# Kernel optimization log

Measured on AMD Instinct MI355X. Metric: run time of the kernel, lower is better.

## Reference

```python
import jax, jax.numpy as jnp
import numpy as np

BATCH, SEQ, EMBED = 8, 1024, 2048
HEADS, LATENT = 16, 512
HEAD_DIM = EMBED // HEADS            # 128
NOPE = HEAD_DIM // 4                 # 32 (qk_rope_dim=96 is even, no adjust)
ROPE_D = HEAD_DIM - NOPE             # 96
THETA = 10000.0


def _rope_tables(seq_len):
    # matches torch: freqs over arange(0, rope_dim, 2)/rope_dim
    freqs = 1.0 / THETA ** (jnp.arange(0, ROPE_D, 2, dtype=jnp.float32) / ROPE_D)
    emb = jnp.arange(seq_len, dtype=jnp.float32)[:, None] * freqs[None, :]  # [S, ROPE_D//2]
    return jnp.cos(emb), jnp.sin(emb)


def _apply_rope(x, cos, sin):
    # x: [B,H,S,D]; cos/sin: [S,D//2]. NOTE: original concatenates halves (non-interleaved output).
    xe, xo = x[..., ::2], x[..., 1::2]
    return jnp.concatenate([xe * cos - xo * sin, xo * cos + xe * sin], axis=-1)


def setup_inputs() -> dict:
    key = jax.random.key(0)
    ks = jax.random.split(key, 5)
    x = jax.random.normal(ks[0], (BATCH, SEQ, EMBED), jnp.float32)
    Wq = jax.random.normal(ks[1], (EMBED, EMBED), jnp.float32) * 0.02
    Wkv_down = jax.random.normal(ks[2], (EMBED, LATENT), jnp.float32) * 0.02
    Wk_up = jax.random.normal(ks[3], (LATENT, EMBED), jnp.float32) * 0.02
    Wv_up = jax.random.normal(ks[4], (LATENT, EMBED), jnp.float32) * 0.02
    return {"x": x, "Wq": Wq, "Wkv_down": Wkv_down, "Wk_up": Wk_up, "Wv_up": Wv_up}


def reference(x, Wq, Wkv_down, Wk_up, Wv_up):
    B, S, E = x.shape
    # projections (weights stored [in, out], equivalent to nn.Linear math)
    q = (x @ Wq).reshape(B, S, HEADS, HEAD_DIM).transpose(0, 2, 1, 3)   # [B,H,S,D]
    q_nope, q_rope = q[..., :NOPE], q[..., NOPE:]
    c_kv = x @ Wkv_down                                                  # [B,S,latent]
    k = (c_kv @ Wk_up).reshape(B, S, HEADS, HEAD_DIM).transpose(0, 2, 1, 3)
    v = (c_kv @ Wv_up).reshape(B, S, HEADS, HEAD_DIM).transpose(0, 2, 1, 3)
    k_nope, k_rope = k[..., :NOPE], k[..., NOPE:]

    cos, sin = _rope_tables(S)
    q_rope = _apply_rope(q_rope, cos, sin)
    k_rope = _apply_rope(k_rope, cos, sin)

    qf = jnp.concatenate([q_nope, q_rope], axis=-1)
    kf = jnp.concatenate([k_nope, k_rope], axis=-1)

    scale = jnp.float32(1.0 / np.sqrt(HEAD_DIM))
    scores = jnp.einsum('bhqd,bhkd->bhqk', qf, kf) * scale
    causal = jnp.triu(jnp.ones((S, S), dtype=bool), k=1)  # past_length=0
    scores = jnp.where(causal, -jnp.inf, scores)
    weights = jax.nn.softmax(scores, axis=-1)
    out = jnp.einsum('bhqk,bhkd->bhqd', weights, v)
    return out.transpose(0, 2, 1, 3).reshape(B, S, E)
```

## Files before the change

### kernel.cpp

```cpp
#include <hip/hip_runtime.h>
#include <stdint.h>

typedef unsigned short u16;
typedef __bf16 bf16x8 __attribute__((ext_vector_type(8)));
typedef float    f32x4 __attribute__((ext_vector_type(4)));
typedef unsigned short u16x8 __attribute__((ext_vector_type(8)));
typedef unsigned short u16x4 __attribute__((ext_vector_type(4)));

#define BB 8
#define SS 1024
#define EE 2048
#define HH 16
#define DD 128

__device__ __forceinline__ u16 f2bf(float f){
  union { float f; unsigned u; } v; v.f = f;
  unsigned r = v.u + 0x7FFFu + ((v.u >> 16) & 1u);
  return (u16)(r >> 16);
}
__device__ __forceinline__ float bf2f(u16 h){
  union { unsigned u; float f; } v; v.u = ((unsigned)h) << 16;
  return v.f;
}
__device__ __forceinline__ bf16x8 ld8(const u16* p){
  return __builtin_bit_cast(bf16x8, *(const u16x8*)p);
}

typedef __attribute__((address_space(1))) const unsigned int gas_u32;
typedef __attribute__((address_space(3))) unsigned int las_u32;
__device__ __forceinline__ void g2l16(const u16* g, u16* l){
  __builtin_amdgcn_global_load_lds((gas_u32*)g, (las_u32*)l, 16, 0, 0);
}

#define BARRIER() asm volatile("s_barrier" ::: "memory")
#define VMC(n)    asm volatile("s_waitcnt vmcnt(" #n ")" ::: "memory")

__global__ __launch_bounds__(256) void cvt_f32_bf16(const float* __restrict__ in,
                                                    u16* __restrict__ out, int n){
  int i = (blockIdx.x*256 + threadIdx.x)*8;
  if (i >= n) return;
  float4 v0 = *(const float4*)(in + i);
  float4 v1 = *(const float4*)(in + i + 4);
  u16x8 o;
  o[0]=f2bf(v0.x); o[1]=f2bf(v0.y); o[2]=f2bf(v0.z); o[3]=f2bf(v0.w);
  o[4]=f2bf(v1.x); o[5]=f2bf(v1.y); o[6]=f2bf(v1.z); o[7]=f2bf(v1.w);
  *(u16x8*)(out + i) = o;
}

__global__ __launch_bounds__(256) void transposeW(const float* __restrict__ W,
                                                  u16* __restrict__ Wt, int K, int N){
  __shared__ float t[32][33];
  int c = threadIdx.x & 31, r = threadIdx.x >> 5;
  int bx = blockIdx.x, by = blockIdx.y;
  #pragma unroll
  for (int i = 0; i < 32; i += 8)
    t[r+i][c] = W[(size_t)(by*32 + r + i)*N + bx*32 + c];
  __syncthreads();
  #pragma unroll
  for (int i = 0; i < 32; i += 8)
    Wt[(size_t)(bx*32 + r + i)*K + by*32 + c] = f2bf(t[c][r+i]);
}

__global__ __launch_bounds__(256) void rope_tables(float* __restrict__ cosb,
                                                   float* __restrict__ sinb){
  int i = blockIdx.x*256 + threadIdx.x;
  if (i >= SS*48) return;
  int s = i / 48, j = i % 48;
  float freq = powf(10000.0f, -((float)(2*j)) / 96.0f);
  float e = (float)s * freq;
  cosb[i] = cosf(e);
  sinb[i] = sinf(e);
}

__global__ __launch_bounds__(256) void rope_apply2(u16* __restrict__ qp,
                                                   u16* __restrict__ kp,
                                                   const float* __restrict__ cosb,
                                                   const float* __restrict__ sinb){
  u16* base = blockIdx.y ? kp : qp;
  int t = blockIdx.x*256 + threadIdx.x;
  int row = t >> 4, h = t & 15, s = row & (SS-1);
  u16* p = base + (size_t)row*EE + h*DD + 32;
  float e[48], o[48];
  #pragma unroll
  for (int c = 0; c < 12; c++){
    u16x8 v = *(const u16x8*)(p + c*8);
    #pragma unroll
    for (int j = 0; j < 4; j++){
      e[c*4 + j] = bf2f(v[2*j]);
      o[c*4 + j] = bf2f(v[2*j+1]);
    }
  }
  u16 ob[96];
  #pragma unroll
  for (int j = 0; j < 48; j++){
    float cs = cosb[s*48 + j], sn = sinb[s*48 + j];
    ob[j]      = f2bf(e[j]*cs - o[j]*sn);
    ob[48 + j] = f2bf(o[j]*cs + e[j]*sn);
  }
  #pragma unroll
  for (int c = 0; c < 12; c++)
    *(u16x8*)(p + c*8) = *(const u16x8*)(ob + c*8);
}

__global__ __launch_bounds__(256) void gemm_bt(const u16* __restrict__ A,
    const u16* __restrict__ Bt, u16* __restrict__ C, int M, int N, int K){
  __shared__ u16 Al[128*32];
  __shared__ u16 Bl[128*32];
  const int tid = threadIdx.x;
  const int lane = tid & 63, w = tid >> 6;
  const int wr = w >> 1, wc = w & 1;
  const int l15 = lane & 15, l4 = lane >> 4;
  const int bm = blockIdx.y*128, bn = blockIdx.x*128;
  const int srow = tid >> 2;
  const int skc  = (tid & 3) * 8;
  const u16* ga = A  + (size_t)(bm + srow)*K + skc;
  const u16* gb = Bt + (size_t)(bn + srow)*K + skc;
  u16* la = Al + w*512;
  u16* lb = Bl + w*512;
  f32x4 acc[4][4] = {};
  for (int k0 = 0; k0 < K; k0 += 32){
    __syncthreads();
    g2l16(ga + k0,          la);
    g2l16(ga + 64*K + k0,   la + 2048);
    g2l16(gb + k0,          lb);
    g2l16(gb + 64*K + k0,   lb + 2048);
    __syncthreads();
    bf16x8 af[4], bfr[4];
    #pragma unroll
    for (int m = 0; m < 4; m++) af[m]  = ld8(Al + (wr*64 + m*16 + l15)*32 + l4*8);
    #pragma unroll
    for (int n = 0; n < 4; n++) bfr[n] = ld8(Bl + (wc*64 + n*16 + l15)*32 + l4*8);
    #pragma unroll
    for (int m = 0; m < 4; m++)
      #pragma unroll
      for (int n = 0; n < 4; n++)
        acc[m][n] = __builtin_amdgcn_mfma_f32_16x16x32_bf16(af[m], bfr[n], acc[m][n], 0, 0, 0);
  }
  #pragma unroll
  for (int m = 0; m < 4; m++)
    #pragma unroll
    for (int n = 0; n < 4; n++)
      #pragma unroll
      for (int r = 0; r < 4; r++){
        int row = bm + wr*64 + m*16 + l4*4 + r;
        int col = bn + wc*64 + n*16 + l15;
        C[(size_t)row*N + col] = f2bf(acc[m][n][r]);
      }
}

#define AFR(buf, mf, ks) ld8(&AL[buf][wr][((mf)*16 + l15)*64 + ((((ks)*4 + l4) ^ r7) << 3)])
#define BFR(buf, nf, ks) ld8(&BL[buf][wc>>1][(((wc&1)*64 + (nf)*16 + l15))*64 + ((((ks)*4 + l4) ^ r7) << 3)])

#define STAGE_A(buf, h, kt) stage2(aRow, (h), (kt), K, &AL[buf][h][0], wj0)
#define STAGE_B(buf, h, kt) stage2(bRow, (h), (kt), K, &BL[buf][h][0], wj0)

__device__ __forceinline__ void stage2(const u16* rowbase, int h, int kt, int K,
                                       u16* lds, int wj0){
  const u16* g = rowbase + (size_t)h*128*K + kt*64;
  g2l16(g,               lds + wj0*512);
  g2l16(g + (size_t)8*K, lds + wj0*512 + 512);
}

#define PHASE(buf, q, LOADB, STAGE, VM) do{                                        \
  bf16x8 a00 = AFR(buf, 2*(q)  , 0);                                              \
  bf16x8 a01 = AFR(buf, 2*(q)  , 1);                                              \
  bf16x8 a10 = AFR(buf, 2*(q)+1, 0);                                              \
  bf16x8 a11 = AFR(buf, 2*(q)+1, 1);                                              \
  if (LOADB){                                                                      \
    _Pragma("unroll")                                                              \
    for (int nf = 0; nf < 4; nf++){ bq[nf][0]=BFR(buf,nf,0); bq[nf][1]=BFR(buf,nf,1); } \
  }                                                                                \
  STAGE;                                                                           \
  if (VM) VMC(4);                                                                  \
  BARRIER();                                                                       \
  __builtin_amdgcn_s_setprio(1);                                                   \
  _Pragma("unroll")                                                                \
  for (int nf = 0; nf < 4; nf++){                                                  \
    acc[2*(q)][nf]   = __builtin_amdgcn_mfma_f32_16x16x32_bf16(a00, bq[nf][0], acc[2*(q)][nf],0,0,0);   \
    acc[2*(q)+1][nf] = __builtin_amdgcn_mfma_f32_16x16x32_bf16(a10, bq[nf][0], acc[2*(q)+1][nf],0,0,0); \
  }                                                                                \
  _Pragma("unroll")                                                                \
  for (int nf = 0; nf < 4; nf++){                                                  \
    acc[2*(q)][nf]   = __builtin_amdgcn_mfma_f32_16x16x32_bf16(a01, bq[nf][1], acc[2*(q)][nf],0,0,0);   \
    acc[2*(q)+1][nf] = __builtin_amdgcn_mfma_f32_16x16x32_bf16(a11, bq[nf][1], acc[2*(q)+1][nf],0,0,0); \
  }                                                                                \
  __builtin_amdgcn_s_setprio(0);                                                   \
  BARRIER();                                                                       \
  __builtin_amdgcn_sched_barrier(0);                                               \
}while(0)

__global__ __launch_bounds__(512, 2) void gemm8(const u16* __restrict__ A,
    const u16* __restrict__ Bt, u16* __restrict__ C0, u16* __restrict__ C1,
    int K, int Nout, int nsplit, int vt){
  __shared__ u16 AL[2][2][128*64];
  __shared__ u16 BL[2][2][128*64];
  const int tid = threadIdx.x, lane = tid & 63, w = tid >> 6;
  const int wr = w >> 2, wc = w & 3;
  const int l15 = lane & 15, l4 = lane >> 4;
  const int r7 = l15 & 7;
  const int bm = blockIdx.y*256, bn = blockIdx.x*256;
  const int wj0 = w*2;
  const int cswz = (lane & 7) ^ (lane >> 3);
  const u16* aRow = A  + (size_t)(bm + wj0*8 + (lane>>3))*K + cswz*8;
  const u16* bRow = Bt + (size_t)(bn + wj0*8 + (lane>>3))*K + cswz*8;

  const int nkt = K >> 6;
  const int niter = nkt >> 1;

  STAGE_A(0, 0, 0); STAGE_A(0, 1, 0);
  STAGE_B(0, 0, 0); STAGE_B(0, 1, 0);
  STAGE_B(1, 0, 1); STAGE_B(1, 1, 1);
  VMC(4);
  BARRIER();

  f32x4 acc[8][4] = {};
  bf16x8 bq[4][2];

  for (int it = 0; it < niter; ++it){
    const int kto = 2*it + 1;
    int kt2 = 2*it + 2; if (kt2 >= nkt) kt2 -= nkt;
    int kt3 = 2*it + 3; if (kt3 >= nkt) kt3 -= nkt;
    PHASE(0, 0, 1, STAGE_A(1, 0, kto), 0);
    PHASE(0, 1, 0, STAGE_A(1, 1, kto), 0);
    PHASE(0, 2, 0, STAGE_B(0, 0, kt2), 0);
    PHASE(0, 3, 0, STAGE_B(0, 1, kt2), 1);
    PHASE(1, 0, 1, STAGE_A(0, 0, kt2), 0);
    PHASE(1, 1, 0, STAGE_A(0, 1, kt2), 0);
    PHASE(1, 2, 0, STAGE_B(1, 0, kt3), 0);
    PHASE(1, 3, 0, STAGE_B(1, 1, kt3), 1);
  }
  asm volatile("s_waitcnt vmcnt(0)" ::: "memory");

  if (vt && bn >= nsplit){
    const int bcol = bn - nsplit;
    #pragma unroll
    for (int mf = 0; mf < 8; mf++)
      #pragma unroll
      for (int nf = 0; nf < 4; nf++){
        int row0 = bm + wr*128 + mf*16 + l4*4;
        int col  = bcol + wc*64 + nf*16 + l15;
        int bh = (row0 >> 10)*16 + (col >> 7);
        int d  = col & 127;
        int s  = row0 & 1023;
        u16x4 pk;
        #pragma unroll
        for (int r = 0; r < 4; r++) pk[r] = f2bf(acc[mf][nf][r]);
        *(u16x4*)(C1 + (((size_t)(bh*128 + d)) << 10) + s) = pk;
      }
  } else {
    u16* Cd = (bn < nsplit) ? C0 : C1;
    const int bcol = (bn < nsplit) ? bn : bn - nsplit;
    #pragma unroll
    for (int mf = 0; mf < 8; mf++)
      #pragma unroll
      for (int nf = 0; nf < 4; nf++)
        #pragma unroll
        for (int r = 0; r < 4; r++){
          int row = bm + wr*128 + mf*16 + l4*4 + r;
          int col = bcol + wc*64 + nf*16 + l15;
          Cd[(size_t)row*Nout + col] = f2bf(acc[mf][nf][r]);
        }
  }
}

#define PLW 40

__global__ __launch_bounds__(512) void attn(const u16* __restrict__ qp,
                                            const u16* __restrict__ kp,
                                            const u16* __restrict__ vpT,
                                            float* __restrict__ out){
  __shared__ u16 Kl[2][64*128];
  __shared__ u16 Vl[2][128*64];
  __shared__ u16 Pl[8][16*PLW];
  const int tid = threadIdx.x, lane = tid & 63, w = tid >> 6;
  const int l15 = lane & 15, l4 = lane >> 4;
  const int qt = 7 - blockIdx.y;
  const int bh = blockIdx.x;
  const int b = bh >> 4, h = bh & 15;
  const int qbase = qt*128;
  const int qmin = qbase + w*16;
  const int qg = qmin + l15;
  const float c = 0.12751920700948998f;
  const float THR = 62.7f;

  const size_t rowq = (size_t)(b*SS + qg)*EE + h*DD;
  bf16x8 qf[4];
  #pragma unroll
  for (int kk = 0; kk < 4; kk++) qf[kk] = ld8(qp + rowq + kk*32 + l4*8);
  #pragma unroll
  for (int kk = 0; kk < 4; kk++) asm volatile("" : "+v"(qf[kk]));

  f32x4 ao[8] = {};
  float mi = -3e38f, li = 0.0f;

  const int ntiles = 2*qt + 2;
  const int vcc = lane & 7;

  #pragma unroll
  for (int q = 0; q < 2; q++){
    int r = w*8 + q*4 + (lane>>4);
    g2l16(kp + (size_t)(b*SS + r)*EE + h*DD + (((lane&15) ^ (r&7))<<3),
          &Kl[0][0] + w*1024 + q*512);
    int d = w*16 + q*8 + (lane>>3);
    g2l16(vpT + (size_t)(bh*DD + d)*SS + ((vcc ^ (d&7))<<3),
          &Vl[0][0] + w*1024 + q*512);
  }

  for (int t = 0; t < ntiles; t++){
    const int kv0 = t*64;
    const int buf = t & 1;
    {
      const int kvn = (t + 1 < ntiles) ? kv0 + 64 : kv0;
      #pragma unroll
      for (int q = 0; q < 2; q++){
        int r = w*8 + q*4 + (lane>>4);
        g2l16(kp + (size_t)(b*SS + kvn + r)*EE + h*DD + (((lane&15) ^ (r&7))<<3),
              &Kl[buf^1][0] + w*1024 + q*512);
        int d = w*16 + q*8 + (lane>>3);
        g2l16(vpT + (size_t)(bh*DD + d)*SS + kvn + ((vcc ^ (d&7))<<3),
              &Vl[buf^1][0] + w*1024 + q*512);
      }
    }
    VMC(4);
    BARRIER();

    if (kv0 <= qmin + 15){
      float sv[4][4];
      __builtin_amdgcn_s_setprio(1);
      #pragma unroll
      for (int nt = 0; nt < 4; nt++){
        f32x4 sacc = {};
        #pragma unroll
        for (int kk = 0; kk < 4; kk++){
          bf16x8 kf = ld8(&Kl[buf][0] + (nt*16 + l15)*128 + (((kk*4 + l4) ^ (l15&7))<<3));
          sacc = __builtin_amdgcn_mfma_f32_16x16x32_bf16(kf, qf[kk], sacc, 0, 0, 0);
        }
        #pragma unroll
        for (int r = 0; r < 4; r++) sv[nt][r] = sacc[r];
      }
      __builtin_amdgcn_s_setprio(0);
      if (kv0 + 63 > qmin){
        #pragma unroll
        for (int nt = 0; nt < 4; nt++)
          #pragma unroll
          for (int r = 0; r < 4; r++){
            int kg = kv0 + nt*16 + l4*4 + r;
            if (kg > qg) sv[nt][r] = -3e38f;
          }
      }
      float mx = sv[0][0];
      #pragma unroll
      for (int nt = 0; nt < 4; nt++)
        #pragma unroll
        for (int r = 0; r < 4; r++) mx = fmaxf(mx, sv[nt][r]);
      mx = fmaxf(mx, __shfl_xor(mx, 16));
      mx = fmaxf(mx, __shfl_xor(mx, 32));
      if (__any(mx > mi + THR)){
        float mnew = fmaxf(mi, mx);
        float alpha = __builtin_amdgcn_exp2f((mi - mnew)*c);
        li *= alpha;
        #pragma unroll
        for (int n8 = 0; n8 < 8; n8++) ao[n8] *= alpha;
        mi = mnew;
      }
      const float mnc = mi*c;
      float pout[4][4];
      float rs = 0.0f;
      #pragma unroll
      for (int nt = 0; nt < 4; nt++)
        #pragma unroll
        for (int r = 0; r < 4; r++){
          float pv = __builtin_amdgcn_exp2f(__builtin_fmaf(sv[nt][r], c, -mnc));
          pout[nt][r] = pv; rs += pv;
        }
      rs += __shfl_xor(rs, 16);
      rs += __shfl_xor(rs, 32);
      li += rs;
      #pragma unroll
      for (int kk = 0; kk < 2; kk++){
        #pragma unroll
        for (int ntl = 0; ntl < 2; ntl++){
          int nt = kk*2 + ntl;
          u16x4 pk;
          #pragma unroll
          for (int r = 0; r < 4; r++) pk[r] = f2bf(pout[nt][r]);
          *(u16x4*)(&Pl[w][l15*PLW + ntl*16 + l4*4]) = pk;
        }
        bf16x8 pa = ld8(&Pl[w][l15*PLW + l4*8]);
        __builtin_amdgcn_s_setprio(1);
        #pragma unroll
        for (int n8 = 0; n8 < 8; n8++){
          bf16x8 vf = ld8(&Vl[buf][0] + (n8*16 + l15)*64 + (((kk*4 + l4) ^ (l15&7))<<3));
          ao[n8] = __builtin_amdgcn_mfma_f32_16x16x32_bf16(vf, pa, ao[n8], 0, 0, 0);
        }
        __builtin_amdgcn_s_setprio(0);
      }
    }
    BARRIER();
  }
  asm volatile("s_waitcnt vmcnt(0)" ::: "memory");

  const float inv = 1.0f / li;
  const size_t orow = (size_t)(b*SS + qg)*EE + h*DD;
  #pragma unroll
  for (int n8 = 0; n8 < 8; n8++){
    f32x4 o = ao[n8]*inv;
    *(float4*)(out + orow + n8*16 + l4*4) = __builtin_bit_cast(float4, o);
  }
}

extern "C" void kernel_launch(void* const* d_in, const int* in_sizes, int n_in,
                              void* d_out, int out_size, void* d_ws, size_t ws_size,
                              hipStream_t stream){
  const float* x    = (const float*)d_in[0];
  const float* Wq   = (const float*)d_in[1];
  const float* Wkvd = (const float*)d_in[2];
  const float* Wku  = (const float*)d_in[3];
  const float* Wvu  = (const float*)d_in[4];
  float* out = (float*)d_out;
  char* ws = (char*)d_ws;

  u16*   xb    = (u16*)  (ws);
  u16*   WqT   = (u16*)  (ws +  33554432);
  u16*   WkvdT = (u16*)  (ws +  41943040);
  u16*   WkuT  = (u16*)  (ws +  44040192);
  u16*   WvuT  = (u16*)  (ws +  46137344);
  float* cosb  = (float*)(ws +  48234496);
  float* sinb  = (float*)(ws +  48431104);
  u16*   qp    = (u16*)  (ws +  48627712);
  u16*   ckv   = (u16*)  (ws +  82182144);
  u16*   kp    = (u16*)  (ws +  90570752);
  u16*   vpT   = (u16*)  (ws + 124125184);

  cvt_f32_bf16<<<(BB*SS*EE)/(256*8), 256, 0, stream>>>(x, xb, BB*SS*EE);
  transposeW<<<dim3(EE/32,  EE/32), 256, 0, stream>>>(Wq,   WqT,   EE,  EE);
  transposeW<<<dim3(512/32, EE/32), 256, 0, stream>>>(Wkvd, WkvdT, EE,  512);
  transposeW<<<dim3(EE/32, 512/32), 256, 0, stream>>>(Wku,  WkuT,  512, EE);
  transposeW<<<dim3(EE/32, 512/32), 256, 0, stream>>>(Wvu,  WvuT,  512, EE);
  rope_tables<<<(SS*48 + 255)/256, 256, 0, stream>>>(cosb, sinb);

  gemm8<<<dim3(EE/256, (BB*SS)/256), 512, 0, stream>>>(xb, WqT, qp, qp, EE, EE, EE, 0);
  gemm_bt<<<dim3(512/128, (BB*SS)/128), 256, 0, stream>>>(xb, WkvdT, ckv, BB*SS, 512, EE);
  gemm8<<<dim3(4096/256, (BB*SS)/256), 512, 0, stream>>>(ckv, WkuT, kp, vpT, 512, EE, EE, 1);

  rope_apply2<<<dim3((BB*SS*HH)/256, 2), 256, 0, stream>>>(qp, kp, cosb, sinb);

  attn<<<dim3(BB*HH, SS/128), 512, 0, stream>>>(qp, kp, vpT, out);
}
```

Baseline: 306.8 us.

## Fuse Q and KV-down projections into one GEMM and triple-buffer A tiles

After: 306.2 us. About the same (-0.2%).

```diff
diff --git a/kernel.cpp b/kernel.cpp
--- a/kernel.cpp
+++ b/kernel.cpp
@@ -102,57 +102,11 @@
     *(u16x8*)(p + c*8) = *(const u16x8*)(ob + c*8);
 }
 
-__global__ __launch_bounds__(256) void gemm_bt(const u16* __restrict__ A,
-    const u16* __restrict__ Bt, u16* __restrict__ C, int M, int N, int K){
-  __shared__ u16 Al[128*32];
-  __shared__ u16 Bl[128*32];
-  const int tid = threadIdx.x;
-  const int lane = tid & 63, w = tid >> 6;
-  const int wr = w >> 1, wc = w & 1;
-  const int l15 = lane & 15, l4 = lane >> 4;
-  const int bm = blockIdx.y*128, bn = blockIdx.x*128;
-  const int srow = tid >> 2;
-  const int skc  = (tid & 3) * 8;
-  const u16* ga = A  + (size_t)(bm + srow)*K + skc;
-  const u16* gb = Bt + (size_t)(bn + srow)*K + skc;
-  u16* la = Al + w*512;
-  u16* lb = Bl + w*512;
-  f32x4 acc[4][4] = {};
-  for (int k0 = 0; k0 < K; k0 += 32){
-    __syncthreads();
-    g2l16(ga + k0,          la);
-    g2l16(ga + 64*K + k0,   la + 2048);
-    g2l16(gb + k0,          lb);
-    g2l16(gb + 64*K + k0,   lb + 2048);
-    __syncthreads();
-    bf16x8 af[4], bfr[4];
-    #pragma unroll
-    for (int m = 0; m < 4; m++) af[m]  = ld8(Al + (wr*64 + m*16 + l15)*32 + l4*8);
-    #pragma unroll
-    for (int n = 0; n < 4; n++) bfr[n] = ld8(Bl + (wc*64 + n*16 + l15)*32 + l4*8);
-    #pragma unroll
-    for (int m = 0; m < 4; m++)
-      #pragma unroll
-      for (int n = 0; n < 4; n++)
-        acc[m][n] = __builtin_amdgcn_mfma_f32_16x16x32_bf16(af[m], bfr[n], acc[m][n], 0, 0, 0);
-  }
-  #pragma unroll
-  for (int m = 0; m < 4; m++)
-    #pragma unroll
-    for (int n = 0; n < 4; n++)
-      #pragma unroll
-      for (int r = 0; r < 4; r++){
-        int row = bm + wr*64 + m*16 + l4*4 + r;
-        int col = bn + wc*64 + n*16 + l15;
-        C[(size_t)row*N + col] = f2bf(acc[m][n][r]);
-      }
-}
-
-#define AFR(buf, mf, ks) ld8(&AL[buf][wr][((mf)*16 + l15)*64 + ((((ks)*4 + l4) ^ r7) << 3)])
-#define BFR(buf, nf, ks) ld8(&BL[buf][wc>>1][(((wc&1)*64 + (nf)*16 + l15))*64 + ((((ks)*4 + l4) ^ r7) << 3)])
-
-#define STAGE_A(buf, h, kt) stage2(aRow, (h), (kt), K, &AL[buf][h][0], wj0)
-#define STAGE_B(buf, h, kt) stage2(bRow, (h), (kt), K, &BL[buf][h][0], wj0)
+#define AFRP(APTR, mf, ks) ld8((APTR) + wr*8192 + ((mf)*16 + l15)*64 + ((((ks)*4 + l4) ^ r7) << 3))
+#define BFR(bb, nf, ks)    ld8(&BL[bb][wc>>1][(((wc&1)*64 + (nf)*16 + l15))*64 + ((((ks)*4 + l4) ^ r7) << 3)])
+
+#define STAGE_AP(ptr, h, kt) stage2(aRow, (h), (kt), K, (ptr) + (h)*8192, wj0)
+#define STAGE_B(bb, h, kt)   stage2(bRow, (h), (kt), K, &BL[bb][h][0], wj0)
 
 __device__ __forceinline__ void stage2(const u16* rowbase, int h, int kt, int K,
                                        u16* lds, int wj0){
@@ -161,17 +115,17 @@
   g2l16(g + (size_t)8*K, lds + wj0*512 + 512);
 }
 
-#define PHASE(buf, q, LOADB, STAGE, VM) do{                                        \
-  bf16x8 a00 = AFR(buf, 2*(q)  , 0);                                              \
-  bf16x8 a01 = AFR(buf, 2*(q)  , 1);                                              \
-  bf16x8 a10 = AFR(buf, 2*(q)+1, 0);                                              \
-  bf16x8 a11 = AFR(buf, 2*(q)+1, 1);                                              \
+#define PHASE(APTR, bb, q, LOADB, STAGE, DOVM) do{                                 \
+  bf16x8 a00 = AFRP(APTR, 2*(q)  , 0);                                            \
+  bf16x8 a01 = AFRP(APTR, 2*(q)  , 1);                                            \
+  bf16x8 a10 = AFRP(APTR, 2*(q)+1, 0);                                            \
+  bf16x8 a11 = AFRP(APTR, 2*(q)+1, 1);                                            \
   if (LOADB){                                                                      \
     _Pragma("unroll")                                                              \
-    for (int nf = 0; nf < 4; nf++){ bq[nf][0]=BFR(buf,nf,0); bq[nf][1]=BFR(buf,nf,1); } \
+    for (int nf = 0; nf < 4; nf++){ bq[nf][0]=BFR(bb,nf,0); bq[nf][1]=BFR(bb,nf,1); } \
   }                                                                                \
   STAGE;                                                                           \
-  if (VM) VMC(4);                                                                  \
+  if (DOVM) VMC(8);                                                                \
   BARRIER();                                                                       \
   __builtin_amdgcn_s_setprio(1);                                                   \
   _Pragma("unroll")                                                                \
@@ -191,8 +145,8 @@
 
 __global__ __launch_bounds__(512, 2) void gemm8(const u16* __restrict__ A,
     const u16* __restrict__ Bt, u16* __restrict__ C0, u16* __restrict__ C1,
-    int K, int Nout, int nsplit, int vt){
-  __shared__ u16 AL[2][2][128*64];
+    int K, int Nout0, int Nout1, int nsplit, int vt){
+  __shared__ u16 AL[3][16384];
   __shared__ u16 BL[2][2][128*64];
   const int tid = threadIdx.x, lane = tid & 63, w = tid >> 6;
   const int wr = w >> 2, wc = w & 3;
@@ -207,9 +161,12 @@
   const int nkt = K >> 6;
   const int niter = nkt >> 1;
 
-  STAGE_A(0, 0, 0); STAGE_A(0, 1, 0);
-  STAGE_B(0, 0, 0); STAGE_B(0, 1, 0);
-  STAGE_B(1, 0, 1); STAGE_B(1, 1, 1);
+  u16 *pA0 = &AL[0][0], *pA1 = &AL[1][0], *pA2 = &AL[2][0];
+
+  STAGE_AP(pA0, 0, 0); STAGE_AP(pA0, 1, 0);
+  STAGE_AP(pA1, 0, 1); STAGE_AP(pA1, 1, 1);
+  STAGE_B(0, 0, 0);    STAGE_B(0, 1, 0);
+  STAGE_B(1, 0, 1);    STAGE_B(1, 1, 1);
   VMC(4);
   BARRIER();
 
@@ -217,17 +174,17 @@
   bf16x8 bq[4][2];
 
   for (int it = 0; it < niter; ++it){
-    const int kto = 2*it + 1;
     int kt2 = 2*it + 2; if (kt2 >= nkt) kt2 -= nkt;
     int kt3 = 2*it + 3; if (kt3 >= nkt) kt3 -= nkt;
-    PHASE(0, 0, 1, STAGE_A(1, 0, kto), 0);
-    PHASE(0, 1, 0, STAGE_A(1, 1, kto), 0);
-    PHASE(0, 2, 0, STAGE_B(0, 0, kt2), 0);
-    PHASE(0, 3, 0, STAGE_B(0, 1, kt2), 1);
-    PHASE(1, 0, 1, STAGE_A(0, 0, kt2), 0);
-    PHASE(1, 1, 0, STAGE_A(0, 1, kt2), 0);
-    PHASE(1, 2, 0, STAGE_B(1, 0, kt3), 0);
-    PHASE(1, 3, 0, STAGE_B(1, 1, kt3), 1);
+    PHASE(pA0, 0, 0, 1, STAGE_AP(pA2, 0, kt2), 0);
+    PHASE(pA0, 0, 1, 0, STAGE_AP(pA2, 1, kt2), 0);
+    PHASE(pA0, 0, 2, 0, STAGE_B(0, 0, kt2),    0);
+    PHASE(pA0, 0, 3, 0, STAGE_B(0, 1, kt2),    1);
+    PHASE(pA1, 1, 0, 1, STAGE_AP(pA0, 0, kt3), 0);
+    PHASE(pA1, 1, 1, 0, STAGE_AP(pA0, 1, kt3), 0);
+    PHASE(pA1, 1, 2, 0, STAGE_B(1, 0, kt3),    0);
+    PHASE(pA1, 1, 3, 0, STAGE_B(1, 1, kt3),    1);
+    u16* t = pA0; pA0 = pA2; pA2 = pA1; pA1 = t;
   }
   asm volatile("s_waitcnt vmcnt(0)" ::: "memory");
 
@@ -249,6 +206,7 @@
       }
   } else {
     u16* Cd = (bn < nsplit) ? C0 : C1;
+    const int No = (bn < nsplit) ? Nout0 : Nout1;
     const int bcol = (bn < nsplit) ? bn : bn - nsplit;
     #pragma unroll
     for (int mf = 0; mf < 8; mf++)
@@ -258,7 +216,7 @@
         for (int r = 0; r < 4; r++){
           int row = bm + wr*128 + mf*16 + l4*4 + r;
           int col = bcol + wc*64 + nf*16 + l15;
-          Cd[(size_t)row*Nout + col] = f2bf(acc[mf][nf][r]);
+          Cd[(size_t)row*No + col] = f2bf(acc[mf][nf][r]);
         }
   }
 }
@@ -439,9 +397,10 @@
   transposeW<<<dim3(EE/32, 512/32), 256, 0, stream>>>(Wvu,  WvuT,  512, EE);
   rope_tables<<<(SS*48 + 255)/256, 256, 0, stream>>>(cosb, sinb);
 
-  gemm8<<<dim3(EE/256, (BB*SS)/256), 512, 0, stream>>>(xb, WqT, qp, qp, EE, EE, EE, 0);
-  gemm_bt<<<dim3(512/128, (BB*SS)/128), 256, 0, stream>>>(xb, WkvdT, ckv, BB*SS, 512, EE);
-  gemm8<<<dim3(4096/256, (BB*SS)/256), 512, 0, stream>>>(ckv, WkuT, kp, vpT, 512, EE, EE, 1);
+  gemm8<<<dim3(2560/256, (BB*SS)/256), 512, 0, stream>>>(xb, WqT, qp, ckv,
+                                                         EE, EE, 512, EE, 0);
+  gemm8<<<dim3(4096/256, (BB*SS)/256), 512, 0, stream>>>(ckv, WkuT, kp, vpT,
+                                                         512, EE, 0, EE, 1);
 
   rope_apply2<<<dim3((BB*SS*HH)/256, 2), 256, 0, stream>>>(qp, kp, cosb, sinb);
 
```
